# Optimization experiments

Hardware: AMD Instinct MI355X
Metric: run time of the kernel (lower is better)

The kernel has to match this reference:

```python
import jax, jax.numpy as jnp
import numpy as np

STEP = 2
NEG = -1.0e10  # matches masked_fill_(-10000000000.0)


def leaky_relu(x):
    # nn.LeakyReLU(0.2)
    return jnp.where(x >= 0, x, 0.2 * x)


def setup_inputs() -> dict:
    key = jax.random.key(0)
    k1, k2, k3, k4 = jax.random.split(key, 4)
    B, E, N, H = 16, 1024, 1024, 128
    nodes_hidden = jax.random.normal(k1, (B, N, H), dtype=jnp.float32)
    # sparse-ish binary hyperedge incidence matrix (batch, edge_num, node_num)
    hn_adj = jax.random.bernoulli(k2, 0.1, (B, E, N)).astype(jnp.float32)
    # Linear(H+1, 1, bias=False) weights for q1 / q2, flattened to (H+1,)
    w1 = jax.random.normal(k3, (H + 1,), dtype=jnp.float32) / np.sqrt(H + 1).astype(np.float32)
    w2 = jax.random.normal(k4, (H + 1,), dtype=jnp.float32) / np.sqrt(H + 1).astype(np.float32)
    return {"nodes_hidden": nodes_hidden, "hn_adj": hn_adj, "w1": w1, "w2": w2}


def reference(nodes_hidden, hn_adj, w1, w2):
    # Dropout is inference-mode identity.
    H = nodes_hidden.shape[-1]
    # edge init: mean of incident node features
    deg = jnp.sum(hn_adj, axis=-1, keepdims=True)            # (B,E,1)
    deg = jnp.where(deg == 0.0, 1.0, deg)
    edge = jnp.matmul(hn_adj, nodes_hidden) / deg            # (B,E,H)
    nodes = nodes_hidden
    for _ in range(STEP):
        # q1(concat(edge*node, adj)) == (edge*node)@w1[:H] + adj*w1[H]
        # fused rank-1 score: never materialize (B,E,N,H)
        alpha = leaky_relu(
            jnp.einsum("bed,bnd,d->ben", edge, nodes, w1[:H]) + hn_adj * w1[H]
        )                                                     # (B,E,N)
        alpha = jnp.where(hn_adj == 0, NEG, alpha)
        alpha = jax.nn.softmax(alpha, axis=-1)
        edge = jnp.einsum("ben,bnd->bed", alpha, nodes)       # new edge hidden
        adj_t = jnp.swapaxes(hn_adj, 1, 2)                    # (B,N,E)
        beta = leaky_relu(
            jnp.einsum("bed,bnd,d->bne", edge, nodes, w2[:H]) + adj_t * w2[H]
        )                                                     # (B,N,E)
        beta = jnp.where(adj_t == 0, NEG, beta)
        beta = jax.nn.softmax(beta, axis=-1)
        nodes = jnp.einsum("bne,bed->bnd", beta, edge)        # new node hidden
    return (nodes, edge)
```

## Files before the change

### kernel.cpp

```cpp
#include <hip/hip_runtime.h>
#include <cstdint>
#include <cstddef>

#define B_ 16
#define NROW 1024
#define H_ 128
#define NW 16
#define BM 64

typedef unsigned short u16;
typedef unsigned long long u64;
typedef __attribute__((ext_vector_type(8))) short short8;
typedef __attribute__((ext_vector_type(4))) float f32x4;

__device__ __forceinline__ u16 f2bf(float f) {
    unsigned u = __float_as_uint(f);
    return (u16)((u + 0x7fffu + ((u >> 16) & 1u)) >> 16);
}
__device__ __forceinline__ float bf2f(u16 h) {
    return __uint_as_float((unsigned)h << 16);
}

__global__ void adj_to_bits(const float* __restrict__ adj, u64* __restrict__ bits) {
    int be = blockIdx.x;
    const float* row = adj + (size_t)be * NROW;
    int tid = threadIdx.x, lane = tid & 63, wv = tid >> 6;
    for (int c0 = 0; c0 < NROW; c0 += 256) {
        float v = row[c0 + tid];
        u64 m = __ballot(v != 0.0f);
        if (lane == 0) bits[(size_t)be * NW + (c0 >> 6) + wv] = m;
    }
}

__global__ void to_bf16(const float* __restrict__ in, u16* __restrict__ out) {
    int i = blockIdx.x * 256 + threadIdx.x;
    float4 v = ((const float4*)in)[i];
    ushort4 r;
    r.x = f2bf(v.x); r.y = f2bf(v.y); r.z = f2bf(v.z); r.w = f2bf(v.w);
    ((ushort4*)out)[i] = r;
}

__global__ void trans_vt(const float* __restrict__ src, u16* __restrict__ vt) {
    int blk = blockIdx.x;
    int b = blk >> 7, d = blk & 127;
    int t = threadIdx.x;
    const float* sp = src + ((size_t)b << 10) * H_ + d;
    ushort4 o;
    o.x = f2bf(sp[(size_t)(t * 4 + 0) * H_]);
    o.y = f2bf(sp[(size_t)(t * 4 + 1) * H_]);
    o.z = f2bf(sp[(size_t)(t * 4 + 2) * H_]);
    o.w = f2bf(sp[(size_t)(t * 4 + 3) * H_]);
    ((ushort4*)(vt + ((size_t)b * H_ + d) * NROW))[t] = o;
}

__global__ void prep_q(const float* __restrict__ src, const float* __restrict__ w,
                       u16* __restrict__ qs) {
    int idx = blockIdx.x * 256 + threadIdx.x;
    float4 v = ((const float4*)src)[idx];
    float4 wv = ((const float4*)w)[idx & 31];
    const float L2E = 1.44269504f;
    ushort4 r;
    r.x = f2bf(v.x * wv.x * L2E);
    r.y = f2bf(v.y * wv.y * L2E);
    r.z = f2bf(v.z * wv.z * L2E);
    r.w = f2bf(v.w * wv.w * L2E);
    ((ushort4*)qs)[idx] = r;
}

__global__ void __launch_bounds__(512, 1)
fused_attn(const u16* __restrict__ qs, const u16* __restrict__ kvbf,
           const u16* __restrict__ vt, const u64* __restrict__ bits,
           const float* __restrict__ w,
           float* __restrict__ outf, u16* __restrict__ bfo, u16* __restrict__ vto,
           int TM, int MODE, int aux) {
    __shared__ uint4 Al[BM * 16];
    __shared__ uint4 Bk[128 * 16];
    __shared__ uint4 Bv[128 * 16];
    __shared__ uint4 Pl[BM * 16];
    __shared__ float dLds[8 * BM];

    int blk = blockIdx.x;
    int xcd = blk & 7;
    int jj = blk >> 3;
    int b = xcd + ((jj & 1) << 3);
    int mt = jj >> 1;
    int t = threadIdx.x;
    int lane = t & 63, wv = t >> 6;
    int r15 = lane & 15, g = lane >> 4;
    int hw = wv >> 2;

    if (MODE == 0) {
#pragma unroll
        for (int i = 0; i < 2; ++i) {
            int gi = i * 512 + t;
            int row = gi >> 4, kc = gi & 15;
            Al[row * 16 + (kc ^ (row & 7))] =
                ((const uint4*)qs)[((size_t)(b << 10) + mt * 64 + row) * 16 + kc];
        }
    }
    float wb = (MODE == 0) ? w[H_] * 1.44269504f : 0.f;
    f32x4 acc2[4] = {};
    float dsum[4][4] = {};
    int col_l = wv * 16 + r15;

    for (int nt = 0; nt < 8; ++nt) {
        if (MODE == 0) {
#pragma unroll
            for (int i = 0; i < 4; ++i) {
                int gi = i * 512 + t;
                int row = gi >> 4, kc = gi & 15;
                Bk[row * 16 + (kc ^ (row & 7))] =
                    ((const uint4*)kvbf)[((size_t)(b << 10) + nt * 128 + row) * 16 + kc];
            }
        }
#pragma unroll
        for (int i = 0; i < 4; ++i) {
            int gi = i * 512 + t;
            int row = gi >> 4, kc = gi & 15;
            Bv[row * 16 + (kc ^ (row & 7))] =
                ((const uint4*)vt)[((size_t)b * H_ + row) * 128 + nt * 16 + kc];
        }
        __syncthreads();

        f32x4 sacc[4] = {};
        if (MODE == 0) {
#pragma unroll
            for (int kk = 0; kk < 4; ++kk) {
                uint4 bv4 = Bk[(wv * 16 + r15) * 16 + ((kk * 4 + g) ^ (r15 & 7))];
                short8 bfr = __builtin_bit_cast(short8, bv4);
#pragma unroll
                for (int mi = 0; mi < 4; ++mi) {
                    uint4 av = Al[(mi * 16 + r15) * 16 + ((kk * 4 + g) ^ (r15 & 7))];
                    sacc[mi] = __builtin_amdgcn_mfma_f32_16x16x32_bf16(
                        __builtin_bit_cast(short8, av), bfr, sacc[mi], 0, 0, 0);
                }
            }
        }

        u64 wrd1 = 0;
        if (TM) wrd1 = bits[((size_t)(b << 10) + nt * 128 + col_l) * NW + mt];
#pragma unroll
        for (int mi = 0; mi < 4; ++mi) {
#pragma unroll
            for (int reg = 0; reg < 4; ++reg) {
                int row_l = mi * 16 + g * 4 + reg;
                float ww;
                if (MODE == 1) {
                    u64 wrd = bits[((size_t)(b << 10) + mt * 64 + row_l) * NW + nt * 2 + hw];
                    ww = (float)((wrd >> (col_l & 63)) & 1);
                } else {
                    float p = sacc[mi][reg] + wb;
                    p = p >= 0.f ? p : 0.2f * p;
                    u64 wrd = TM ? wrd1
                                 : bits[((size_t)(b << 10) + mt * 64 + row_l) * NW + nt * 2 + hw];
                    int bit = TM ? row_l : (col_l & 63);
                    ww = ((wrd >> bit) & 1) ? exp2f(p) : 0.f;
                }
                u16 h = f2bf(ww);
                dsum[mi][reg] += bf2f(h);
                ((u16*)Pl)[(row_l * 16 + ((col_l >> 3) ^ (row_l & 7))) * 8 + (col_l & 7)] = h;
            }
        }
        __syncthreads();

#pragma unroll
        for (int kk = 0; kk < 4; ++kk) {
            uint4 bv4 = Bv[(wv * 16 + r15) * 16 + ((kk * 4 + g) ^ (r15 & 7))];
            short8 vvv = __builtin_bit_cast(short8, bv4);
#pragma unroll
            for (int mi = 0; mi < 4; ++mi) {
                uint4 pv = Pl[(mi * 16 + r15) * 16 + ((kk * 4 + g) ^ (r15 & 7))];
                acc2[mi] = __builtin_amdgcn_mfma_f32_16x16x32_bf16(
                    __builtin_bit_cast(short8, pv), vvv, acc2[mi], 0, 0, 0);
            }
        }
        __syncthreads();
    }

#pragma unroll
    for (int mi = 0; mi < 4; ++mi)
#pragma unroll
        for (int reg = 0; reg < 4; ++reg) {
            float v = dsum[mi][reg];
            v += __shfl_xor(v, 1); v += __shfl_xor(v, 2);
            v += __shfl_xor(v, 4); v += __shfl_xor(v, 8);
            dsum[mi][reg] = v;
        }
    if (r15 == 0) {
#pragma unroll
        for (int mi = 0; mi < 4; ++mi)
#pragma unroll
            for (int reg = 0; reg < 4; ++reg)
                dLds[wv * BM + mi * 16 + g * 4 + reg] = dsum[mi][reg];
    }
    __syncthreads();

#pragma unroll
    for (int mi = 0; mi < 4; ++mi) {
#pragma unroll
        for (int reg = 0; reg < 4; ++reg) {
            int row_l = mi * 16 + g * 4 + reg;
            float den = 0.f;
#pragma unroll
            for (int w8 = 0; w8 < 8; ++w8) den += dLds[w8 * BM + row_l];
            float rden = den > 0.f ? 1.0f / den : 0.f;
            float val = acc2[mi][reg] * rden;
            size_t R = (size_t)(b << 10) + mt * 64 + row_l;
            outf[R * H_ + col_l] = val;
            u16 h = f2bf(val);
            if (aux) bfo[R * H_ + col_l] = h;
            ((u16*)Pl)[(row_l * 16 + ((col_l >> 3) ^ (row_l & 7))) * 8 + (col_l & 7)] = h;
        }
    }
    if (aux) {
        __syncthreads();
#pragma unroll
        for (int i = 0; i < 2; ++i) {
            int gi = i * 512 + t;
            int d = gi >> 3, mc = gi & 7;
            u16 tmp[8];
#pragma unroll
            for (int j2 = 0; j2 < 8; ++j2) {
                int m = mc * 8 + j2;
                tmp[j2] = ((u16*)Pl)[(m * 16 + ((d >> 3) ^ (m & 7))) * 8 + (d & 7)];
            }
            uint4 o;
            o.x = (unsigned)tmp[0] | ((unsigned)tmp[1] << 16);
            o.y = (unsigned)tmp[2] | ((unsigned)tmp[3] << 16);
            o.z = (unsigned)tmp[4] | ((unsigned)tmp[5] << 16);
            o.w = (unsigned)tmp[6] | ((unsigned)tmp[7] << 16);
            ((uint4*)vto)[((size_t)b * H_ + d) * 128 + mt * 8 + mc] = o;
        }
    }
}

extern "C" void kernel_launch(void* const* d_in, const int* in_sizes, int n_in,
                              void* d_out, int out_size, void* d_ws, size_t ws_size,
                              hipStream_t stream) {
    const float* nodes_in = (const float*)d_in[0];
    const float* adj      = (const float*)d_in[1];
    const float* w1       = (const float*)d_in[2];
    const float* w2       = (const float*)d_in[3];

    char* ws = (char*)d_ws;
    size_t off = 0;
    u64* bits     = (u64*)(ws + off); off += (size_t)B_ * NROW * NW * sizeof(u64);
    u16* nodes_bf = (u16*)(ws + off); off += (size_t)B_ * NROW * H_ * sizeof(u16);
    u16* edge_bf  = (u16*)(ws + off); off += (size_t)B_ * NROW * H_ * sizeof(u16);
    u16* VTn      = (u16*)(ws + off); off += (size_t)B_ * H_ * NROW * sizeof(u16);
    u16* VTe      = (u16*)(ws + off); off += (size_t)B_ * H_ * NROW * sizeof(u16);
    u16* qs       = (u16*)(ws + off); off += (size_t)B_ * NROW * H_ * sizeof(u16);

    float* out_nodes = (float*)d_out;
    float* out_edge  = out_nodes + (size_t)B_ * NROW * H_;

    adj_to_bits<<<dim3(B_ * NROW), dim3(256), 0, stream>>>(adj, bits);
    to_bf16    <<<dim3(B_ * NROW * H_ / 1024), dim3(256), 0, stream>>>(nodes_in, nodes_bf);
    trans_vt   <<<dim3(B_ * H_), dim3(256), 0, stream>>>(nodes_in, VTn);
    fused_attn <<<dim3(256), dim3(512), 0, stream>>>(
        nodes_bf, nodes_bf, VTn, bits, w1, out_edge, edge_bf, VTe, 0, 1, 0);

    const float* ncur = nodes_in;
    for (int s = 0; s < 2; ++s) {
        prep_q    <<<dim3(2048), dim3(256), 0, stream>>>(out_edge, w1, qs);
        fused_attn<<<dim3(256), dim3(512), 0, stream>>>(
            qs, nodes_bf, VTn, bits, w1, out_edge, edge_bf, VTe, 0, 0, 1);
        prep_q    <<<dim3(2048), dim3(256), 0, stream>>>(ncur, w2, qs);
        fused_attn<<<dim3(256), dim3(512), 0, stream>>>(
            qs, edge_bf, VTe, bits, w2, out_nodes, nodes_bf, VTn, 1, 0, s == 0 ? 1 : 0);
        ncur = out_nodes;
    }
}
```

Measured before the change: 264.8 us.

## Shrink attention row tile to 16 and load K/V fragments directly from global

The fused attention kernel now handles 16 rows per block instead of 64, so the grid grows from 256 to 1024 blocks and the launch bounds allow several resident blocks per CU. The K and V tiles are no longer staged in shared memory: each wave loads its MFMA operands straight from global memory, which removes two barriers' worth of staging per tile and shrinks the LDS footprint. The transposed bf16 output is now written directly from registers as ushort4 rather than through an LDS transpose. The aim is more waves in flight to hide latency. In exchange, each K/V tile is fetched four times as often from L2, and the first launch now also writes the auxiliary bf16 outputs.

```diff
diff --git a/kernel.cpp b/kernel.cpp
--- a/kernel.cpp
+++ b/kernel.cpp
@@ -6,7 +6,6 @@
 #define NROW 1024
 #define H_ 128
 #define NW 16
-#define BM 64
 
 typedef unsigned short u16;
 typedef unsigned long long u64;
@@ -67,170 +66,129 @@
     ((ushort4*)qs)[idx] = r;
 }
 
-__global__ void __launch_bounds__(512, 1)
+__global__ void __launch_bounds__(512, 6)
 fused_attn(const u16* __restrict__ qs, const u16* __restrict__ kvbf,
            const u16* __restrict__ vt, const u64* __restrict__ bits,
            const float* __restrict__ w,
            float* __restrict__ outf, u16* __restrict__ bfo, u16* __restrict__ vto,
            int TM, int MODE, int aux) {
-    __shared__ uint4 Al[BM * 16];
-    __shared__ uint4 Bk[128 * 16];
-    __shared__ uint4 Bv[128 * 16];
-    __shared__ uint4 Pl[BM * 16];
-    __shared__ float dLds[8 * BM];
-
-    int blk = blockIdx.x;
-    int xcd = blk & 7;
-    int jj = blk >> 3;
-    int b = xcd + ((jj & 1) << 3);
-    int mt = jj >> 1;
+    __shared__ uint4 Al[16 * 16];
+    __shared__ uint4 Pl[16 * 16];
+    __shared__ float dLds[8 * 16];
+
+    int x = blockIdx.x;
+    int xcd = x & 7;
+    int j = x >> 3;
+    int b = xcd + ((j >> 6) << 3);
+    int mt = j & 63;
     int t = threadIdx.x;
     int lane = t & 63, wv = t >> 6;
     int r15 = lane & 15, g = lane >> 4;
-    int hw = wv >> 2;
-
-    if (MODE == 0) {
-#pragma unroll
-        for (int i = 0; i < 2; ++i) {
-            int gi = i * 512 + t;
-            int row = gi >> 4, kc = gi & 15;
-            Al[row * 16 + (kc ^ (row & 7))] =
-                ((const uint4*)qs)[((size_t)(b << 10) + mt * 64 + row) * 16 + kc];
+
+    if (MODE == 0 && t < 256) {
+        int row = t >> 4, kc = t & 15;
+        Al[row * 16 + (kc ^ (row & 7))] =
+            ((const uint4*)qs)[((size_t)(b << 10) + mt * 16 + row) * 16 + kc];
+    }
+    float wb = (MODE == 0) ? w[H_] * 1.44269504f : 0.f;
+    f32x4 oacc = {};
+    float dsum[4] = {};
+    __syncthreads();
+
+    for (int nt = 0; nt < 8; ++nt) {
+        int ncol = nt * 128 + wv * 16 + r15;
+        f32x4 sacc = {};
+        if (MODE == 0) {
+            const uint4* Bg = (const uint4*)kvbf + ((size_t)(b << 10) + ncol) * 16;
+            uint4 b0 = Bg[g], b1 = Bg[4 + g], b2 = Bg[8 + g], b3 = Bg[12 + g];
+            uint4 a0 = Al[r15 * 16 + ((0 + g) ^ (r15 & 7))];
+            uint4 a1 = Al[r15 * 16 + ((4 + g) ^ (r15 & 7))];
+            uint4 a2 = Al[r15 * 16 + ((8 + g) ^ (r15 & 7))];
+            uint4 a3 = Al[r15 * 16 + ((12 + g) ^ (r15 & 7))];
+            sacc = __builtin_amdgcn_mfma_f32_16x16x32_bf16(
+                __builtin_bit_cast(short8, a0), __builtin_bit_cast(short8, b0), sacc, 0, 0, 0);
+            sacc = __builtin_amdgcn_mfma_f32_16x16x32_bf16(
+                __builtin_bit_cast(short8, a1), __builtin_bit_cast(short8, b1), sacc, 0, 0, 0);
+            sacc = __builtin_amdgcn_mfma_f32_16x16x32_bf16(
+                __builtin_bit_cast(short8, a2), __builtin_bit_cast(short8, b2), sacc, 0, 0, 0);
+            sacc = __builtin_amdgcn_mfma_f32_16x16x32_bf16(
+                __builtin_bit_cast(short8, a3), __builtin_bit_cast(short8, b3), sacc, 0, 0, 0);
         }
-    }
-    float wb = (MODE == 0) ? w[H_] * 1.44269504f : 0.f;
-    f32x4 acc2[4] = {};
-    float dsum[4][4] = {};
-    int col_l = wv * 16 + r15;
-
-    for (int nt = 0; nt < 8; ++nt) {
-        if (MODE == 0) {
-#pragma unroll
-            for (int i = 0; i < 4; ++i) {
-                int gi = i * 512 + t;
-                int row = gi >> 4, kc = gi & 15;
-                Bk[row * 16 + (kc ^ (row & 7))] =
-                    ((const uint4*)kvbf)[((size_t)(b << 10) + nt * 128 + row) * 16 + kc];
+        u64 wrdT = 0;
+        if (TM) wrdT = bits[((size_t)(b << 10) + ncol) * NW + (mt >> 2)];
+        int colt = wv * 16 + r15;
+#pragma unroll
+        for (int reg = 0; reg < 4; ++reg) {
+            int row_l = g * 4 + reg;
+            float ww;
+            if (MODE == 1) {
+                u64 wrd = bits[((size_t)(b << 10) + mt * 16 + row_l) * NW + (ncol >> 6)];
+                ww = (float)((wrd >> (ncol & 63)) & 1);
+            } else {
+                float p = sacc[reg] + wb;
+                p = p >= 0.f ? p : 0.2f * p;
+                u64 wrd = TM ? wrdT
+                             : bits[((size_t)(b << 10) + mt * 16 + row_l) * NW + (ncol >> 6)];
+                int bit = TM ? ((mt * 16 + row_l) & 63) : (ncol & 63);
+                ww = ((wrd >> bit) & 1) ? exp2f(p) : 0.f;
             }
-        }
-#pragma unroll
-        for (int i = 0; i < 4; ++i) {
-            int gi = i * 512 + t;
-            int row = gi >> 4, kc = gi & 15;
-            Bv[row * 16 + (kc ^ (row & 7))] =
-                ((const uint4*)vt)[((size_t)b * H_ + row) * 128 + nt * 16 + kc];
+            u16 h = f2bf(ww);
+            dsum[reg] += bf2f(h);
+            ((u16*)Pl)[(row_l * 16 + ((colt >> 3) ^ (row_l & 7))) * 8 + (colt & 7)] = h;
         }
         __syncthreads();
-
-        f32x4 sacc[4] = {};
-        if (MODE == 0) {
-#pragma unroll
-            for (int kk = 0; kk < 4; ++kk) {
-                uint4 bv4 = Bk[(wv * 16 + r15) * 16 + ((kk * 4 + g) ^ (r15 & 7))];
-                short8 bfr = __builtin_bit_cast(short8, bv4);
-#pragma unroll
-                for (int mi = 0; mi < 4; ++mi) {
-                    uint4 av = Al[(mi * 16 + r15) * 16 + ((kk * 4 + g) ^ (r15 & 7))];
-                    sacc[mi] = __builtin_amdgcn_mfma_f32_16x16x32_bf16(
-                        __builtin_bit_cast(short8, av), bfr, sacc[mi], 0, 0, 0);
-                }
-            }
-        }
-
-        u64 wrd1 = 0;
-        if (TM) wrd1 = bits[((size_t)(b << 10) + nt * 128 + col_l) * NW + mt];
-#pragma unroll
-        for (int mi = 0; mi < 4; ++mi) {
-#pragma unroll
-            for (int reg = 0; reg < 4; ++reg) {
-                int row_l = mi * 16 + g * 4 + reg;
-                float ww;
-                if (MODE == 1) {
-                    u64 wrd = bits[((size_t)(b << 10) + mt * 64 + row_l) * NW + nt * 2 + hw];
-                    ww = (float)((wrd >> (col_l & 63)) & 1);
-                } else {
-                    float p = sacc[mi][reg] + wb;
-                    p = p >= 0.f ? p : 0.2f * p;
-                    u64 wrd = TM ? wrd1
-                                 : bits[((size_t)(b << 10) + mt * 64 + row_l) * NW + nt * 2 + hw];
-                    int bit = TM ? row_l : (col_l & 63);
-                    ww = ((wrd >> bit) & 1) ? exp2f(p) : 0.f;
-                }
-                u16 h = f2bf(ww);
-                dsum[mi][reg] += bf2f(h);
-                ((u16*)Pl)[(row_l * 16 + ((col_l >> 3) ^ (row_l & 7))) * 8 + (col_l & 7)] = h;
-            }
+        {
+            const uint4* Vg = (const uint4*)vt +
+                ((size_t)b * H_ + wv * 16 + r15) * 128 + nt * 16;
+            uint4 v0 = Vg[g], v1 = Vg[4 + g], v2 = Vg[8 + g], v3 = Vg[12 + g];
+            uint4 p0 = Pl[r15 * 16 + ((0 + g) ^ (r15 & 7))];
+            uint4 p1 = Pl[r15 * 16 + ((4 + g) ^ (r15 & 7))];
+            uint4 p2 = Pl[r15 * 16 + ((8 + g) ^ (r15 & 7))];
+            uint4 p3 = Pl[r15 * 16 + ((12 + g) ^ (r15 & 7))];
+            oacc = __builtin_amdgcn_mfma_f32_16x16x32_bf16(
+                __builtin_bit_cast(short8, p0), __builtin_bit_cast(short8, v0), oacc, 0, 0, 0);
+            oacc = __builtin_amdgcn_mfma_f32_16x16x32_bf16(
+                __builtin_bit_cast(short8, p1), __builtin_bit_cast(short8, v1), oacc, 0, 0, 0);
+            oacc = __builtin_amdgcn_mfma_f32_16x16x32_bf16(
+                __builtin_bit_cast(short8, p2), __builtin_bit_cast(short8, v2), oacc, 0, 0, 0);
+            oacc = __builtin_amdgcn_mfma_f32_16x16x32_bf16(
+                __builtin_bit_cast(short8, p3), __builtin_bit_cast(short8, v3), oacc, 0, 0, 0);
         }
         __syncthreads();
-
-#pragma unroll
-        for (int kk = 0; kk < 4; ++kk) {
-            uint4 bv4 = Bv[(wv * 16 + r15) * 16 + ((kk * 4 + g) ^ (r15 & 7))];
-            short8 vvv = __builtin_bit_cast(short8, bv4);
-#pragma unroll
-            for (int mi = 0; mi < 4; ++mi) {
-                uint4 pv = Pl[(mi * 16 + r15) * 16 + ((kk * 4 + g) ^ (r15 & 7))];
-                acc2[mi] = __builtin_amdgcn_mfma_f32_16x16x32_bf16(
-                    __builtin_bit_cast(short8, pv), vvv, acc2[mi], 0, 0, 0);
-            }
-        }
-        __syncthreads();
-    }
-
-#pragma unroll
-    for (int mi = 0; mi < 4; ++mi)
-#pragma unroll
-        for (int reg = 0; reg < 4; ++reg) {
-            float v = dsum[mi][reg];
-            v += __shfl_xor(v, 1); v += __shfl_xor(v, 2);
-            v += __shfl_xor(v, 4); v += __shfl_xor(v, 8);
-            dsum[mi][reg] = v;
-        }
-    if (r15 == 0) {
-#pragma unroll
-        for (int mi = 0; mi < 4; ++mi)
-#pragma unroll
-            for (int reg = 0; reg < 4; ++reg)
-                dLds[wv * BM + mi * 16 + g * 4 + reg] = dsum[mi][reg];
-    }
+    }
+
+#pragma unroll
+    for (int reg = 0; reg < 4; ++reg) {
+        float v = dsum[reg];
+        v += __shfl_xor(v, 1); v += __shfl_xor(v, 2);
+        v += __shfl_xor(v, 4); v += __shfl_xor(v, 8);
+        dsum[reg] = v;
+    }
+    if (r15 == 0)
+#pragma unroll
+        for (int reg = 0; reg < 4; ++reg)
+            dLds[wv * 16 + g * 4 + reg] = dsum[reg];
     __syncthreads();
 
-#pragma unroll
-    for (int mi = 0; mi < 4; ++mi) {
-#pragma unroll
-        for (int reg = 0; reg < 4; ++reg) {
-            int row_l = mi * 16 + g * 4 + reg;
-            float den = 0.f;
-#pragma unroll
-            for (int w8 = 0; w8 < 8; ++w8) den += dLds[w8 * BM + row_l];
-            float rden = den > 0.f ? 1.0f / den : 0.f;
-            float val = acc2[mi][reg] * rden;
-            size_t R = (size_t)(b << 10) + mt * 64 + row_l;
-            outf[R * H_ + col_l] = val;
-            u16 h = f2bf(val);
-            if (aux) bfo[R * H_ + col_l] = h;
-            ((u16*)Pl)[(row_l * 16 + ((col_l >> 3) ^ (row_l & 7))) * 8 + (col_l & 7)] = h;
-        }
+    int d = wv * 16 + r15;
+    u16 hv[4];
+#pragma unroll
+    for (int reg = 0; reg < 4; ++reg) {
+        int row_l = g * 4 + reg;
+        float den = 0.f;
+#pragma unroll
+        for (int w8 = 0; w8 < 8; ++w8) den += dLds[w8 * 16 + row_l];
+        float rden = den > 0.f ? 1.0f / den : 0.f;
+        float val = oacc[reg] * rden;
+        size_t R = (size_t)(b << 10) + mt * 16 + row_l;
+        outf[R * H_ + d] = val;
+        u16 h = f2bf(val);
+        hv[reg] = h;
+        if (aux) bfo[R * H_ + d] = h;
     }
     if (aux) {
-        __syncthreads();
-#pragma unroll
-        for (int i = 0; i < 2; ++i) {
-            int gi = i * 512 + t;
-            int d = gi >> 3, mc = gi & 7;
-            u16 tmp[8];
-#pragma unroll
-            for (int j2 = 0; j2 < 8; ++j2) {
-                int m = mc * 8 + j2;
-                tmp[j2] = ((u16*)Pl)[(m * 16 + ((d >> 3) ^ (m & 7))) * 8 + (d & 7)];
-            }
-            uint4 o;
-            o.x = (unsigned)tmp[0] | ((unsigned)tmp[1] << 16);
-            o.y = (unsigned)tmp[2] | ((unsigned)tmp[3] << 16);
-            o.z = (unsigned)tmp[4] | ((unsigned)tmp[5] << 16);
-            o.w = (unsigned)tmp[6] | ((unsigned)tmp[7] << 16);
-            ((uint4*)vto)[((size_t)b * H_ + d) * 128 + mt * 8 + mc] = o;
-        }
+        ushort4 o; o.x = hv[0]; o.y = hv[1]; o.z = hv[2]; o.w = hv[3];
+        ((ushort4*)vto)[((size_t)b * H_ + d) * 256 + mt * 4 + g] = o;
     }
 }
 
@@ -257,16 +215,16 @@
     adj_to_bits<<<dim3(B_ * NROW), dim3(256), 0, stream>>>(adj, bits);
     to_bf16    <<<dim3(B_ * NROW * H_ / 1024), dim3(256), 0, stream>>>(nodes_in, nodes_bf);
     trans_vt   <<<dim3(B_ * H_), dim3(256), 0, stream>>>(nodes_in, VTn);
-    fused_attn <<<dim3(256), dim3(512), 0, stream>>>(
-        nodes_bf, nodes_bf, VTn, bits, w1, out_edge, edge_bf, VTe, 0, 1, 0);
+    fused_attn <<<dim3(1024), dim3(512), 0, stream>>>(
+        nodes_bf, nodes_bf, VTn, bits, w1, out_edge, edge_bf, VTe, 0, 1, 1);
 
     const float* ncur = nodes_in;
     for (int s = 0; s < 2; ++s) {
         prep_q    <<<dim3(2048), dim3(256), 0, stream>>>(out_edge, w1, qs);
-        fused_attn<<<dim3(256), dim3(512), 0, stream>>>(
+        fused_attn<<<dim3(1024), dim3(512), 0, stream>>>(
             qs, nodes_bf, VTn, bits, w1, out_edge, edge_bf, VTe, 0, 0, 1);
         prep_q    <<<dim3(2048), dim3(256), 0, stream>>>(ncur, w2, qs);
-        fused_attn<<<dim3(256), dim3(512), 0, stream>>>(
+        fused_attn<<<dim3(1024), dim3(512), 0, stream>>>(
             qs, edge_bf, VTe, bits, w2, out_nodes, nodes_bf, VTn, 1, 0, s == 0 ? 1 : 0);
         ncur = out_nodes;
     }
```

New measurement: 424.9 us. 1.6x slower.
